# Kernel tuning notes

Measured on AMD Instinct MI355X. Metric: run time of the kernel, lower is better.

## Reference

```python
import jax, jax.numpy as jnp
import numpy as np

GB_TAU = 1.0
_NOISE_KEY = jax.random.key(42)


def setup_inputs() -> dict:
    key = jax.random.key(0)
    kq, kk, kv = jax.random.split(key, 3)
    n_genes, n_latent, d_k, n_cells = 16384, 4096, 64, 1024
    query = jax.random.normal(kq, (n_genes, d_k), dtype=jnp.float32)
    key_t = jax.random.normal(kk, (n_latent, d_k), dtype=jnp.float32)
    value = jax.random.normal(kv, (n_latent, n_cells), dtype=jnp.float32)
    return {"query": query, "key": key_t, "value": value}


def _gumbel_noise(shape, dtype):
    # standard Gumbel(0,1): -log(-log(U)), U ~ Uniform(0,1)
    u = jax.random.uniform(_NOISE_KEY, shape, dtype=dtype,
                           minval=jnp.finfo(dtype).tiny, maxval=1.0)
    return -jnp.log(-jnp.log(u))


def reference(query, key, value):
    d_k = query.shape[-1]
    # [n_genes, n_latent] scaled dot-product scores
    scores = jnp.matmul(query, key.T) / jnp.sqrt(jnp.asarray(d_k, query.dtype))
    # gumbel_softmax(hard=False): softmax((logits + g) / tau, axis=-1)
    g = _gumbel_noise(scores.shape, scores.dtype)
    p_attn = jax.nn.softmax((scores + g) / GB_TAU, axis=-1)
    out = jnp.matmul(p_attn, value)  # [n_genes, n_cells]
    return out, p_attn
```

## Files before the change

kernel.cpp:

```cpp
#include <hip/hip_runtime.h>
#include <cstdint>
#include <cstddef>

#define N_GENES  16384
#define N_LATENT 4096
#define D_K      64
#define N_CELLS  1024

#define NOISE_PARTITIONABLE 1

typedef __attribute__((ext_vector_type(8))) short bf16x8;
typedef __attribute__((ext_vector_type(4))) float f32x4;

__device__ __forceinline__ uint32_t rotl32(uint32_t x, int r) {
  return __builtin_amdgcn_alignbit(x, x, 32 - r);
}

__device__ __forceinline__ void threefry2x32(uint32_t c0, uint32_t c1,
                                             uint32_t& o0, uint32_t& o1) {
  const uint32_t ks0 = 0u, ks1 = 42u, ks2 = 0u ^ 42u ^ 0x1BD11BDAu;
  uint32_t x0 = c0 + ks0;
  uint32_t x1 = c1 + ks1;
#define TFR(r) { x0 += x1; x1 = rotl32(x1, r); x1 ^= x0; }
  TFR(13) TFR(15) TFR(26) TFR(6)
  x0 += ks1; x1 += ks2 + 1u;
  TFR(17) TFR(29) TFR(16) TFR(24)
  x0 += ks2; x1 += ks0 + 2u;
  TFR(13) TFR(15) TFR(26) TFR(6)
  x0 += ks0; x1 += ks1 + 3u;
  TFR(17) TFR(29) TFR(16) TFR(24)
  x0 += ks1; x1 += ks2 + 4u;
  TFR(13) TFR(15) TFR(26) TFR(6)
  x0 += ks2; x1 += ks0 + 5u;
#undef TFR
  o0 = x0; o1 = x1;
}

__device__ __forceinline__ uint32_t rand_bits(uint32_t m) {
#if NOISE_PARTITIONABLE
  uint32_t b0, b1;
  threefry2x32(0u, m, b0, b1);
  return b0 ^ b1;
#else
  const uint32_t h = 1u << 25;
  uint32_t b0, b1;
  if (m < h) { threefry2x32(m, m + h, b0, b1); return b0; }
  else       { threefry2x32(m - h, m, b0, b1); return b1; }
#endif
}

__device__ __forceinline__ float fastlog(float x) {
  float r;
  asm("v_log_f32 %0, %1" : "=v"(r) : "v"(x));
  return r * 0.69314718055994531f;
}

__device__ __forceinline__ float gumbel_noise(uint32_t m) {
  uint32_t bits = rand_bits(m);
  float f = __uint_as_float((bits >> 9) | 0x3f800000u) - 1.0f;
  float u = f + 1.17549435e-38f;
  float t = -fastlog(u);
  return -fastlog(t);
}

__device__ __forceinline__ ushort f2bf(float x) {
  uint32_t u = __float_as_uint(x);
  uint32_t r = (u + 0x7FFFu + ((u >> 16) & 1u)) >> 16;
  return (ushort)r;
}

__device__ __forceinline__ float bf2f(uint32_t us) {
  return __uint_as_float(us << 16);
}

__device__ __forceinline__ uint32_t cvtpk_bf16(float lo, float hi) {
  uint32_t r;
  asm("v_cvt_pk_bf16_f32 %0, %1, %2" : "=v"(r) : "v"(lo), "v"(hi));
  return r;
}

__device__ __forceinline__ int swz(int row, int kcol) {
  return row * 64 + (((kcol >> 3) ^ (row & 7)) << 3) + (kcol & 7);
}

__global__ __launch_bounds__(256) void k_logexp(const float* __restrict__ Q,
                                                const float* __restrict__ Kk,
                                                ushort* __restrict__ Pe,
                                                float* __restrict__ Sp) {
  __shared__ ushort Qh[64 * 64], Ql[64 * 64], Kh[64 * 64], Kl[64 * 64];
  const int t = threadIdx.x;
  const int bm = blockIdx.x, bn = blockIdx.y;
  const float4* Q4 = (const float4*)(Q + ((size_t)bm << 12));
  const float4* K4 = (const float4*)(Kk + ((size_t)bn << 12));
#pragma unroll
  for (int i = 0; i < 4; ++i) {
    int idx = t + (i << 8);
    int r = idx >> 4;
    int k0 = (idx & 15) << 2;
    int sidx = swz(r, k0);
    float4 a = Q4[idx];
    a.x *= 0.125f; a.y *= 0.125f; a.z *= 0.125f; a.w *= 0.125f;
    {
      uint32_t h01 = cvtpk_bf16(a.x, a.y), h23 = cvtpk_bf16(a.z, a.w);
      float lx = a.x - __uint_as_float(h01 << 16);
      float ly = a.y - __uint_as_float(h01 & 0xffff0000u);
      float lz = a.z - __uint_as_float(h23 << 16);
      float lw = a.w - __uint_as_float(h23 & 0xffff0000u);
      uint32_t l01 = cvtpk_bf16(lx, ly), l23 = cvtpk_bf16(lz, lw);
      *(uint2*)&Qh[sidx] = make_uint2(h01, h23);
      *(uint2*)&Ql[sidx] = make_uint2(l01, l23);
    }
    float4 b = K4[idx];
    {
      uint32_t h01 = cvtpk_bf16(b.x, b.y), h23 = cvtpk_bf16(b.z, b.w);
      float lx = b.x - __uint_as_float(h01 << 16);
      float ly = b.y - __uint_as_float(h01 & 0xffff0000u);
      float lz = b.z - __uint_as_float(h23 << 16);
      float lw = b.w - __uint_as_float(h23 & 0xffff0000u);
      uint32_t l01 = cvtpk_bf16(lx, ly), l23 = cvtpk_bf16(lz, lw);
      *(uint2*)&Kh[sidx] = make_uint2(h01, h23);
      *(uint2*)&Kl[sidx] = make_uint2(l01, l23);
    }
  }
  __syncthreads();

  const int l = t & 63, w = t >> 6;
  const int wm = (w >> 1) << 5, wn = (w & 1) << 5;
  const int fr = l & 15;
  const int seg = l >> 4;
  const int koff = seg << 3;
  f32x4 acc[2][2] = {};
#pragma unroll
  for (int kseg = 0; kseg < 2; ++kseg) {
    bf16x8 ah[2], al[2], bh[2], bl[2];
    const int kc = kseg * 32 + koff;
#pragma unroll
    for (int m = 0; m < 2; ++m) {
      int row = wm + m * 16 + fr;
      int sidx = swz(row, kc);
      ah[m] = *(const bf16x8*)&Qh[sidx];
      al[m] = *(const bf16x8*)&Ql[sidx];
    }
#pragma unroll
    for (int n = 0; n < 2; ++n) {
      int row = wn + n * 16 + fr;
      int sidx = swz(row, kc);
      bh[n] = *(const bf16x8*)&Kh[sidx];
      bl[n] = *(const bf16x8*)&Kl[sidx];
    }
#pragma unroll
    for (int m = 0; m < 2; ++m)
#pragma unroll
      for (int n = 0; n < 2; ++n) {
        acc[m][n] = __builtin_amdgcn_mfma_f32_16x16x32_bf16(
            ah[m], bh[n], acc[m][n], 0, 0, 0);
        acc[m][n] = __builtin_amdgcn_mfma_f32_16x16x32_bf16(
            ah[m], bl[n], acc[m][n], 0, 0, 0);
        acc[m][n] = __builtin_amdgcn_mfma_f32_16x16x32_bf16(
            al[m], bh[n], acc[m][n], 0, 0, 0);
      }
  }

  const float LOG2E = 1.44269504088896340f;
  const float NLN2 = -0.69314718055994531f;
  const int gr0 = (bm << 6) + wm + (seg << 2);
  const int gc0 = (bn << 6) + wn + fr;
  float sloc[2][4] = {};
#pragma unroll
  for (int m = 0; m < 2; ++m)
#pragma unroll
    for (int n = 0; n < 2; ++n) {
      int col = gc0 + n * 16;
      uint32_t mbase = (uint32_t)(gr0 + m * 16) * 4096u + (uint32_t)col;
      float e[4];
#pragma unroll
      for (int j = 0; j < 4; ++j) {
        uint32_t bits = rand_bits(mbase + (uint32_t)j * 4096u);
        float f = __uint_as_float((bits >> 9) | 0x3f800000u) - 1.0f;
        float u = f + 1.17549435e-38f;
        float lgu;
        asm("v_log_f32 %0, %1" : "=v"(lgu) : "v"(u));
        float tq = lgu * NLN2;
        float lgt;
        asm("v_log_f32 %0, %1" : "=v"(lgt) : "v"(tq));
        float ee;
        asm("v_exp_f32 %0, %1" : "=v"(ee)
            : "v"(fmaf(acc[m][n][j], LOG2E, -lgt)));
        e[j] = ee;
        sloc[m][j] += ee;
      }
      uint32_t p01 = cvtpk_bf16(e[0], e[1]);
      uint32_t p23 = cvtpk_bf16(e[2], e[3]);
      size_t base = (size_t)(gr0 + m * 16) * 4096 + col;
      Pe[base] = (ushort)p01;
      Pe[base + 4096] = (ushort)(p01 >> 16);
      Pe[base + 2 * 4096] = (ushort)p23;
      Pe[base + 3 * 4096] = (ushort)(p23 >> 16);
    }
  __shared__ float part[64][2];
#pragma unroll
  for (int m = 0; m < 2; ++m)
#pragma unroll
    for (int j = 0; j < 4; ++j) {
      float s = sloc[m][j];
      s += __shfl_xor(s, 1, 64); s += __shfl_xor(s, 2, 64);
      s += __shfl_xor(s, 4, 64); s += __shfl_xor(s, 8, 64);
      if (fr == 0) part[wm + m * 16 + (seg << 2) + j][wn >> 5] = s;
    }
  __syncthreads();
  if (t < 64)
    Sp[((size_t)(bm << 6) + t) * 64 + bn] = part[t][0] + part[t][1];
}

__global__ __launch_bounds__(256) void k_rowinv(const float* __restrict__ Sp,
                                                float* __restrict__ inv) {
  int r = blockIdx.x * 256 + threadIdx.x;
  const float4* s4 = (const float4*)(Sp + (size_t)r * 64);
  float s = 0.f;
#pragma unroll
  for (int i = 0; i < 16; ++i) {
    float4 v = s4[i];
    s += (v.x + v.y) + (v.z + v.w);
  }
  inv[r] = 1.0f / s;
}

__global__ __launch_bounds__(256) void k_vt(const float* __restrict__ V,
                                            ushort* __restrict__ VT) {
  __shared__ ushort tile[64][68];
  const int t = threadIdx.x;
  const int k0 = blockIdx.x << 6, n0 = blockIdx.y << 6;
#pragma unroll
  for (int i = 0; i < 16; ++i) {
    int idx = t + (i << 8);
    int kr = idx >> 6;
    int c = idx & 63;
    tile[c][kr] = f2bf(V[(size_t)(k0 + kr) * 1024 + n0 + c]);
  }
  __syncthreads();
#pragma unroll
  for (int i = 0; i < 8; ++i) {
    int idx = t + (i << 8);
    int n = idx >> 5, kp = idx & 31;
    ushort2 o;
    o.x = tile[n][2 * kp];
    o.y = tile[n][2 * kp + 1];
    ((ushort2*)&VT[(size_t)(n0 + n) * 4096 + k0])[kp] = o;
  }
}

__device__ __forceinline__ void llds16(void* lds, const void* g) {
  __builtin_amdgcn_global_load_lds(
      (const __attribute__((address_space(1))) uint32_t*)g,
      (__attribute__((address_space(3))) uint32_t*)lds, 16, 0, 0);
}

__device__ __forceinline__ void stage_kt(ushort* ldsA, ushort* ldsB,
                                         const ushort* gA, const ushort* gB,
                                         int t) {
#pragma unroll
  for (int i = 0; i < 4; ++i) {
    int cid = (i << 9) + t;
    int row = cid >> 3, g = cid & 7;
    int gs = g ^ (row & 7);
    llds16(ldsA + (size_t)cid * 8, gA + (size_t)row * 4096 + gs * 8);
  }
#pragma unroll
  for (int i = 0; i < 4; ++i) {
    int cid = (i << 9) + t;
    int row = cid >> 3, g = cid & 7;
    int gs = g ^ (row & 7);
    llds16(ldsB + (size_t)cid * 8, gB + (size_t)row * 4096 + gs * 8);
  }
}

__global__ __launch_bounds__(512, 2) void k_pv4(const ushort* __restrict__ Pe,
                                                const ushort* __restrict__ VT,
                                                const float* __restrict__ inv,
                                                float* __restrict__ P,
                                                float* __restrict__ O) {
  __shared__ ushort lds[2][2][256 * 64];
  const int t = threadIdx.x;
  const int b = blockIdx.x;
  const int xcd = b & 7, idx = b >> 3;
  const int by = xcd * 8 + (idx >> 2);
  const int bx = idx & 3;
  const int base_m = by << 8, base_n = bx << 8;
  const int l = t & 63, w = t >> 6;
  const int wm = w >> 2, wn = w & 3;
  const int fr = l & 15, seg = l >> 4;

  const ushort* gA = Pe + (size_t)base_m * 4096;
  const ushort* gB = VT + (size_t)base_n * 4096;

  const int pr_loc = bx * 64 + (t >> 3);
  const int pw_g = t & 7;
  const int pw_off = pr_loc * 64 + ((pw_g ^ (pr_loc & 7)) << 3);
  const int pw_row = base_m + pr_loc;
  const float iv_pw = inv[pw_row];
  float* Pdst = P + (size_t)pw_row * 4096 + pw_g * 8;

  f32x4 acc[8][4] = {};

  stage_kt(lds[0][0], lds[0][1], gA, gB, t);

#define LDA_H(mh)                                                            \
  {                                                                          \
    _Pragma("unroll") for (int m = 0; m < 4; ++m)                            \
        _Pragma("unroll") for (int kk = 0; kk < 2; ++kk) {                   \
      int row = wm * 128 + (mh)*64 + m * 16 + fr;                            \
      a[m][kk] = *(const bf16x8*)&A[row * 64 +                               \
                                    ((((kk << 2) + seg) ^ (row & 7)) << 3)]; \
    }                                                                        \
  }
#define LDB_H(dst, nh)                                                       \
  {                                                                          \
    _Pragma("unroll") for (int n = 0; n < 2; ++n)                            \
        _Pragma("unroll") for (int kk = 0; kk < 2; ++kk) {                   \
      int row = wn * 64 + (nh)*32 + n * 16 + fr;                             \
      dst[n][kk] = *(const bf16x8*)&B[row * 64 +                             \
                                    ((((kk << 2) + seg) ^ (row & 7)) << 3)]; \
    }                                                                        \
  }
#define QUADM(mh, nh, bb)                                                    \
  {                                                                          \
    __builtin_amdgcn_s_setprio(1);                                           \
    _Pragma("unroll") for (int m = 0; m < 4; ++m)                            \
        _Pragma("unroll") for (int n = 0; n < 2; ++n)                        \
            _Pragma("unroll") for (int kk = 0; kk < 2; ++kk)                 \
        acc[(mh)*4 + m][(nh)*2 + n] = __builtin_amdgcn_mfma_f32_16x16x32_bf16( \
            a[m][kk], bb[n][kk], acc[(mh)*4 + m][(nh)*2 + n], 0, 0, 0);      \
    __builtin_amdgcn_s_setprio(0);                                           \
  }

  for (int it = 0; it < 64; ++it) {
    const int slot = it & 1;
    const int ktn = (it < 63) ? it + 1 : it;
    stage_kt(lds[slot ^ 1][0], lds[slot ^ 1][1],
             gA + ktn * 64, gB + ktn * 64, t);
    asm volatile("s_waitcnt vmcnt(8)" ::: "memory");
    __builtin_amdgcn_s_barrier();
    const ushort* A = lds[slot][0];
    const ushort* B = lds[slot][1];
    bf16x8 a[4][2], b0[2][2], b1[2][2];
    LDA_H(0) LDB_H(b0, 0)
    QUADM(0, 0, b0)
    __builtin_amdgcn_s_barrier();
    LDB_H(b1, 1)
    QUADM(0, 1, b1)
    __builtin_amdgcn_s_barrier();
    LDA_H(1)
    QUADM(1, 0, b0)
    __builtin_amdgcn_s_barrier();
    QUADM(1, 1, b1)
    {
      bf16x8 pv_ = *(const bf16x8*)&A[pw_off];
      const uint32_t* pu = (const uint32_t*)&pv_;
      float4 o0, o1;
      uint32_t w0 = pu[0], w1 = pu[1], w2 = pu[2], w3 = pu[3];
      o0.x = bf2f(w0) * iv_pw;        o0.y = bf2f(w0 >> 16) * iv_pw;
      o0.z = bf2f(w1) * iv_pw;        o0.w = bf2f(w1 >> 16) * iv_pw;
      o1.x = bf2f(w2) * iv_pw;        o1.y = bf2f(w2 >> 16) * iv_pw;
      o1.z = bf2f(w3) * iv_pw;        o1.w = bf2f(w3 >> 16) * iv_pw;
      *(float4*)(Pdst + (size_t)it * 64) = o0;
      *(float4*)(Pdst + (size_t)it * 64 + 4) = o1;
    }
    __builtin_amdgcn_s_barrier();
  }

#pragma unroll
  for (int mi = 0; mi < 8; ++mi) {
    int row_ = base_m + wm * 128 + mi * 16 + seg * 4;
#pragma unroll
    for (int j = 0; j < 4; ++j) {
      float iv = inv[row_ + j];
#pragma unroll
      for (int ni = 0; ni < 4; ++ni)
        O[(size_t)(row_ + j) * 1024 + base_n + wn * 64 + ni * 16 + fr] =
            acc[mi][ni][j] * iv;
    }
  }
#undef LDA_H
#undef LDB_H
#undef QUADM
}

__global__ __launch_bounds__(256) void k_logits_raw(const float* __restrict__ Q,
                                                    const float* __restrict__ Kk,
                                                    float* __restrict__ L) {
  __shared__ float Qt[64][68];
  __shared__ float Kt[64][68];
  const int t = threadIdx.x;
  const int bm = blockIdx.x, bn = blockIdx.y;
  const float4* Q4 = (const float4*)(Q + ((size_t)bm << 12));
  const float4* K4 = (const float4*)(Kk + ((size_t)bn << 12));
#pragma unroll
  for (int i = 0; i < 4; ++i) {
    int idx = t + (i << 8);
    int r = idx >> 4;
    int k0 = (idx & 15) << 2;
    float4 a = Q4[idx];
    Qt[k0 + 0][r] = a.x; Qt[k0 + 1][r] = a.y;
    Qt[k0 + 2][r] = a.z; Qt[k0 + 3][r] = a.w;
    float4 b = K4[idx];
    Kt[k0 + 0][r] = b.x; Kt[k0 + 1][r] = b.y;
    Kt[k0 + 2][r] = b.z; Kt[k0 + 3][r] = b.w;
  }
  __syncthreads();
  const int r0 = (t >> 4) << 2;
  const int c0 = (t & 15) << 2;
  float acc[4][4] = {};
#pragma unroll 8
  for (int k = 0; k < 64; ++k) {
    float a[4], b[4];
    *(float4*)a = *(const float4*)&Qt[k][r0];
    *(float4*)b = *(const float4*)&Kt[k][c0];
#pragma unroll
    for (int i = 0; i < 4; ++i)
#pragma unroll
      for (int j = 0; j < 4; ++j)
        acc[i][j] = fmaf(a[i], b[j], acc[i][j]);
  }
  const int gr = (bm << 6) + r0;
  const int gc = (bn << 6) + c0;
#pragma unroll
  for (int i = 0; i < 4; ++i) {
    uint32_t mb = (uint32_t)(gr + i) * 4096u + (uint32_t)gc;
    float4 o;
    o.x = acc[i][0] * 0.125f + gumbel_noise(mb + 0u);
    o.y = acc[i][1] * 0.125f + gumbel_noise(mb + 1u);
    o.z = acc[i][2] * 0.125f + gumbel_noise(mb + 2u);
    o.w = acc[i][3] * 0.125f + gumbel_noise(mb + 3u);
    *(float4*)&L[(size_t)(gr + i) * 4096 + gc] = o;
  }
}

__global__ __launch_bounds__(256) void k_softmax(float* __restrict__ P) {
  const int row = blockIdx.x;
  float* Lr = P + ((size_t)row << 12);
  const int t = threadIdx.x;
  float4 v[4];
#pragma unroll
  for (int i = 0; i < 4; ++i) v[i] = ((const float4*)Lr)[t + (i << 8)];
  float mx = -3.402823466e38f;
#pragma unroll
  for (int i = 0; i < 4; ++i)
    mx = fmaxf(mx, fmaxf(fmaxf(v[i].x, v[i].y), fmaxf(v[i].z, v[i].w)));
#pragma unroll
  for (int o = 1; o < 64; o <<= 1) mx = fmaxf(mx, __shfl_xor(mx, o, 64));
  __shared__ float redm[4];
  __shared__ float reds[4];
  const int lane = t & 63, w = t >> 6;
  if (lane == 0) redm[w] = mx;
  __syncthreads();
  mx = fmaxf(fmaxf(redm[0], redm[1]), fmaxf(redm[2], redm[3]));
  float s = 0.f;
#pragma unroll
  for (int i = 0; i < 4; ++i) {
    v[i].x = expf(v[i].x - mx); v[i].y = expf(v[i].y - mx);
    v[i].z = expf(v[i].z - mx); v[i].w = expf(v[i].w - mx);
    s += (v[i].x + v[i].y) + (v[i].z + v[i].w);
  }
#pragma unroll
  for (int o = 1; o < 64; o <<= 1) s += __shfl_xor(s, o, 64);
  if (lane == 0) reds[w] = s;
  __syncthreads();
  const float inv = 1.0f / (((reds[0] + reds[1]) + (reds[2] + reds[3])));
#pragma unroll
  for (int i = 0; i < 4; ++i) {
    v[i].x *= inv; v[i].y *= inv; v[i].z *= inv; v[i].w *= inv;
    ((float4*)Lr)[t + (i << 8)] = v[i];
  }
}

__global__ __launch_bounds__(256) void k_pv(const float* __restrict__ P,
                                            const float* __restrict__ V,
                                            float* __restrict__ O) {
  __shared__ float Pt[32][132];
  __shared__ float Vs[32][132];
  const int t = threadIdx.x;
  const int base_m = blockIdx.x << 7;
  const int base_n = blockIdx.y << 7;
  const int tr = (t >> 4) << 2;
  const int tc = (t & 15) << 2;
  float acc[2][2][4][4] = {};
  for (int k0 = 0; k0 < N_LATENT; k0 += 32) {
#pragma unroll
    for (int i = 0; i < 4; ++i) {
      int idx = t + (i << 8);
      int m = idx >> 3;
      int kk = (idx & 7) << 2;
      float4 a = *(const float4*)&P[(size_t)(base_m + m) * 4096 + (k0 + kk)];
      Pt[kk + 0][m] = a.x; Pt[kk + 1][m] = a.y;
      Pt[kk + 2][m] = a.z; Pt[kk + 3][m] = a.w;
      int kv = idx >> 5;
      int n4 = (idx & 31) << 2;
      *(float4*)&Vs[kv][n4] =
          *(const float4*)&V[(size_t)(k0 + kv) * 1024 + base_n + n4];
    }
    __syncthreads();
#pragma unroll 4
    for (int k = 0; k < 32; ++k) {
      float a[2][4], b[2][4];
      *(float4*)a[0] = *(const float4*)&Pt[k][tr];
      *(float4*)a[1] = *(const float4*)&Pt[k][tr + 64];
      *(float4*)b[0] = *(const float4*)&Vs[k][tc];
      *(float4*)b[1] = *(const float4*)&Vs[k][tc + 64];
#pragma unroll
      for (int ih = 0; ih < 2; ++ih)
#pragma unroll
        for (int jh = 0; jh < 2; ++jh)
#pragma unroll
          for (int i = 0; i < 4; ++i)
#pragma unroll
            for (int j = 0; j < 4; ++j)
              acc[ih][jh][i][j] =
                  fmaf(a[ih][i], b[jh][j], acc[ih][jh][i][j]);
    }
    __syncthreads();
  }
#pragma unroll
  for (int ih = 0; ih < 2; ++ih)
#pragma unroll
    for (int i = 0; i < 4; ++i) {
      int row = base_m + (ih << 6) + tr + i;
#pragma unroll
      for (int jh = 0; jh < 2; ++jh) {
        float4 o;
        o.x = acc[ih][jh][i][0]; o.y = acc[ih][jh][i][1];
        o.z = acc[ih][jh][i][2]; o.w = acc[ih][jh][i][3];
        *(float4*)&O[(size_t)row * 1024 + base_n + (jh << 6) + tc] = o;
      }
    }
}

extern "C" void kernel_launch(void* const* d_in, const int* in_sizes, int n_in,
                              void* d_out, int out_size, void* d_ws, size_t ws_size,
                              hipStream_t stream) {
  const float* Q = (const float*)d_in[0];
  const float* K = (const float*)d_in[1];
  const float* V = (const float*)d_in[2];
  float* O = (float*)d_out;
  float* P = O + (size_t)N_GENES * N_CELLS;

  const size_t pe_bytes = (size_t)N_GENES * N_LATENT * 2;
  const size_t vt_bytes = (size_t)N_CELLS * N_LATENT * 2;
  const size_t inv_bytes = (size_t)N_GENES * 4;
  const bool fast = ws_size >= pe_bytes + vt_bytes + inv_bytes;

  if (fast) {
    ushort* Pe = (ushort*)d_ws;
    ushort* VT = (ushort*)((char*)d_ws + pe_bytes);
    float* inv = (float*)((char*)d_ws + pe_bytes + vt_bytes);
    float* Sp = P;

    k_logexp<<<dim3(N_GENES / 64, N_LATENT / 64), 256, 0, stream>>>(Q, K, Pe, Sp);
    k_rowinv<<<N_GENES / 256, 256, 0, stream>>>(Sp, inv);
    k_vt<<<dim3(N_LATENT / 64, N_CELLS / 64), 256, 0, stream>>>(V, VT);
    k_pv4<<<256, 512, 0, stream>>>(Pe, VT, inv, P, O);
  } else {
    k_logits_raw<<<dim3(N_GENES / 64, N_LATENT / 64), 256, 0, stream>>>(Q, K, P);
    k_softmax<<<N_GENES, 256, 0, stream>>>(P);
    k_pv<<<dim3(N_GENES / 128, N_CELLS / 128), 256, 0, stream>>>(P, V, O);
  }
}
```

Baseline: 357.7 us.

## Interleave next-tile global-to-LDS loads across MFMA quadrants in PV kernel

The next K-tile's A and B global-to-LDS loads in the PV GEMM are now split into four half-tile issues, one placed between each MFMA quadrant, instead of all being issued at the top of the iteration. The aim is to spread memory traffic through the compute phase and replace the vmcnt(8) wait with a tighter wait at the start of the next iteration. This adds more barriers per iteration and a full drain before the loop begins, and it depends on the fp32 P stores not disturbing the vmcnt accounting.

```diff
diff --git a/kernel.cpp b/kernel.cpp
--- a/kernel.cpp
+++ b/kernel.cpp
@@ -255,26 +255,31 @@
       (__attribute__((address_space(3))) uint32_t*)lds, 16, 0, 0);
 }
 
-__device__ __forceinline__ void stage_kt(ushort* ldsA, ushort* ldsB,
-                                         const ushort* gA, const ushort* gB,
-                                         int t) {
+__device__ __forceinline__ void stage_full(ushort* ldsS, const ushort* gS,
+                                           int t) {
 #pragma unroll
   for (int i = 0; i < 4; ++i) {
     int cid = (i << 9) + t;
     int row = cid >> 3, g = cid & 7;
     int gs = g ^ (row & 7);
-    llds16(ldsA + (size_t)cid * 8, gA + (size_t)row * 4096 + gs * 8);
-  }
-#pragma unroll
-  for (int i = 0; i < 4; ++i) {
+    llds16(ldsS + (size_t)cid * 8, gS + (size_t)row * 4096 + gs * 8);
+  }
+}
+
+__device__ __forceinline__ void stage_half(ushort* ldsS, const ushort* gS,
+                                           int rowoff, int t) {
+#pragma unroll
+  for (int i = 0; i < 2; ++i) {
     int cid = (i << 9) + t;
-    int row = cid >> 3, g = cid & 7;
+    int row = rowoff + (cid >> 3);
+    int g = cid & 7;
     int gs = g ^ (row & 7);
-    llds16(ldsB + (size_t)cid * 8, gB + (size_t)row * 4096 + gs * 8);
-  }
-}
-
-__global__ __launch_bounds__(512, 2) void k_pv4(const ushort* __restrict__ Pe,
+    llds16(ldsS + ((size_t)row * 8 + g) * 8,
+           gS + (size_t)row * 4096 + gs * 8);
+  }
+}
+
+__global__ __launch_bounds__(512, 2) void k_pv5(const ushort* __restrict__ Pe,
                                                 const ushort* __restrict__ VT,
                                                 const float* __restrict__ inv,
                                                 float* __restrict__ P,
@@ -302,7 +307,10 @@
 
   f32x4 acc[8][4] = {};
 
-  stage_kt(lds[0][0], lds[0][1], gA, gB, t);
+  stage_full(lds[0][0], gA, t);
+  stage_full(lds[0][1], gB, t);
+  asm volatile("s_waitcnt vmcnt(0)" ::: "memory");
+  __builtin_amdgcn_s_barrier();
 
 #define LDA_H(mh)                                                            \
   {                                                                          \
@@ -335,22 +343,33 @@
 
   for (int it = 0; it < 64; ++it) {
     const int slot = it & 1;
-    const int ktn = (it < 63) ? it + 1 : it;
-    stage_kt(lds[slot ^ 1][0], lds[slot ^ 1][1],
-             gA + ktn * 64, gB + ktn * 64, t);
-    asm volatile("s_waitcnt vmcnt(8)" ::: "memory");
-    __builtin_amdgcn_s_barrier();
     const ushort* A = lds[slot][0];
     const ushort* B = lds[slot][1];
+    ushort* An = lds[slot ^ 1][0];
+    ushort* Bn = lds[slot ^ 1][1];
+    const ushort* gAn = gA + (it + 1) * 64;
+    const ushort* gBn = gB + (it + 1) * 64;
+    if (it > 0) {
+      asm volatile("s_waitcnt vmcnt(2)" ::: "memory");
+      __builtin_amdgcn_s_barrier();
+    }
     bf16x8 a[4][2], b0[2][2], b1[2][2];
     LDA_H(0) LDB_H(b0, 0)
+    if (it < 63) stage_half(An, gAn, 0, t);
+    __builtin_amdgcn_s_barrier();
     QUADM(0, 0, b0)
     __builtin_amdgcn_s_barrier();
     LDB_H(b1, 1)
+    if (it < 63) stage_half(An, gAn, 128, t);
+    __builtin_amdgcn_s_barrier();
     QUADM(0, 1, b1)
     __builtin_amdgcn_s_barrier();
     LDA_H(1)
+    if (it < 63) stage_half(Bn, gBn, 0, t);
+    __builtin_amdgcn_s_barrier();
     QUADM(1, 0, b0)
+    __builtin_amdgcn_s_barrier();
+    if (it < 63) stage_half(Bn, gBn, 128, t);
     __builtin_amdgcn_s_barrier();
     QUADM(1, 1, b1)
     {
@@ -557,7 +576,7 @@
     k_logexp<<<dim3(N_GENES / 64, N_LATENT / 64), 256, 0, stream>>>(Q, K, Pe, Sp);
     k_rowinv<<<N_GENES / 256, 256, 0, stream>>>(Sp, inv);
     k_vt<<<dim3(N_LATENT / 64, N_CELLS / 64), 256, 0, stream>>>(V, VT);
-    k_pv4<<<256, 512, 0, stream>>>(Pe, VT, inv, P, O);
+    k_pv5<<<256, 512, 0, stream>>>(Pe, VT, inv, P, O);
   } else {
     k_logits_raw<<<dim3(N_GENES / 64, N_LATENT / 64), 256, 0, stream>>>(Q, K, P);
     k_softmax<<<N_GENES, 256, 0, stream>>>(P);
```

Result: faster. 337.6 us (-5.6%).

## Retile PV GEMM to 128x128 blocks with 256 threads and restructured pipeline

Applied to the files above, without the earlier changes.

Replaces the 256x256-tile, 512-thread PV kernel with a 128x128-tile, 256-thread kernel launched over 1024 blocks. Each wave now computes a 64x64 sub-tile, and the block-to-XCD mapping is remapped. The double-buffer pipeline is also changed: it waits for the current tile, then issues the next tile's loads after the barrier. In k_logexp, the row-sum scratch buffer now reuses the Ql LDS buffer, which needs an extra barrier. The aim is better occupancy and load balance across CUs, at the cost of more global reloads of Pe and VT, since smaller tiles give less operand reuse.

```diff
diff --git a/kernel.cpp b/kernel.cpp
--- a/kernel.cpp
+++ b/kernel.cpp
@@ -88,6 +88,7 @@
                                                 ushort* __restrict__ Pe,
                                                 float* __restrict__ Sp) {
   __shared__ ushort Qh[64 * 64], Ql[64 * 64], Kh[64 * 64], Kl[64 * 64];
+  float (*part)[2] = (float(*)[2])Ql;
   const int t = threadIdx.x;
   const int bm = blockIdx.x, bn = blockIdx.y;
   const float4* Q4 = (const float4*)(Q + ((size_t)bm << 12));
@@ -160,6 +161,7 @@
             al[m], bh[n], acc[m][n], 0, 0, 0);
       }
   }
+  __syncthreads();
 
   const float LOG2E = 1.44269504088896340f;
   const float NLN2 = -0.69314718055994531f;
@@ -197,7 +199,6 @@
       Pe[base + 2 * 4096] = (ushort)p23;
       Pe[base + 3 * 4096] = (ushort)(p23 >> 16);
     }
-  __shared__ float part[64][2];
 #pragma unroll
   for (int m = 0; m < 2; ++m)
 #pragma unroll
@@ -255,134 +256,115 @@
       (__attribute__((address_space(3))) uint32_t*)lds, 16, 0, 0);
 }
 
-__device__ __forceinline__ void stage_kt(ushort* ldsA, ushort* ldsB,
-                                         const ushort* gA, const ushort* gB,
+__device__ __forceinline__ void stage128(ushort* ldsS, const ushort* gS,
                                          int t) {
 #pragma unroll
   for (int i = 0; i < 4; ++i) {
-    int cid = (i << 9) + t;
+    int cid = (i << 8) + t;
     int row = cid >> 3, g = cid & 7;
     int gs = g ^ (row & 7);
-    llds16(ldsA + (size_t)cid * 8, gA + (size_t)row * 4096 + gs * 8);
-  }
-#pragma unroll
-  for (int i = 0; i < 4; ++i) {
-    int cid = (i << 9) + t;
-    int row = cid >> 3, g = cid & 7;
-    int gs = g ^ (row & 7);
-    llds16(ldsB + (size_t)cid * 8, gB + (size_t)row * 4096 + gs * 8);
-  }
-}
-
-__global__ __launch_bounds__(512, 2) void k_pv4(const ushort* __restrict__ Pe,
+    llds16(ldsS + (size_t)cid * 8, gS + (size_t)row * 4096 + gs * 8);
+  }
+}
+
+__global__ __launch_bounds__(256, 2) void k_pv6(const ushort* __restrict__ Pe,
                                                 const ushort* __restrict__ VT,
                                                 const float* __restrict__ inv,
                                                 float* __restrict__ P,
                                                 float* __restrict__ O) {
-  __shared__ ushort lds[2][2][256 * 64];
+  __shared__ ushort lds[2][2][128 * 64];
   const int t = threadIdx.x;
   const int b = blockIdx.x;
-  const int xcd = b & 7, idx = b >> 3;
-  const int by = xcd * 8 + (idx >> 2);
-  const int bx = idx & 3;
-  const int base_m = by << 8, base_n = bx << 8;
+  const int Lb = (b & 7) * 128 + (b >> 3);
+  const int by = Lb >> 3, bx = Lb & 7;
+  const int base_m = by << 7, base_n = bx << 7;
   const int l = t & 63, w = t >> 6;
-  const int wm = w >> 2, wn = w & 3;
+  const int wm = (w >> 1) << 6, wn = (w & 1) << 6;
   const int fr = l & 15, seg = l >> 4;
 
   const ushort* gA = Pe + (size_t)base_m * 4096;
   const ushort* gB = VT + (size_t)base_n * 4096;
 
-  const int pr_loc = bx * 64 + (t >> 3);
-  const int pw_g = t & 7;
-  const int pw_off = pr_loc * 64 + ((pw_g ^ (pr_loc & 7)) << 3);
+  const int pr_loc = (bx << 4) + (t >> 4);
+  const int pcg = t & 15;
+  const int pw_ldsoff = pr_loc * 64 + (((pcg >> 1) ^ (pr_loc & 7)) << 3) +
+                        (pcg & 1) * 4;
   const int pw_row = base_m + pr_loc;
   const float iv_pw = inv[pw_row];
-  float* Pdst = P + (size_t)pw_row * 4096 + pw_g * 8;
-
-  f32x4 acc[8][4] = {};
-
-  stage_kt(lds[0][0], lds[0][1], gA, gB, t);
-
-#define LDA_H(mh)                                                            \
-  {                                                                          \
-    _Pragma("unroll") for (int m = 0; m < 4; ++m)                            \
-        _Pragma("unroll") for (int kk = 0; kk < 2; ++kk) {                   \
-      int row = wm * 128 + (mh)*64 + m * 16 + fr;                            \
-      a[m][kk] = *(const bf16x8*)&A[row * 64 +                               \
-                                    ((((kk << 2) + seg) ^ (row & 7)) << 3)]; \
-    }                                                                        \
-  }
-#define LDB_H(dst, nh)                                                       \
-  {                                                                          \
-    _Pragma("unroll") for (int n = 0; n < 2; ++n)                            \
-        _Pragma("unroll") for (int kk = 0; kk < 2; ++kk) {                   \
-      int row = wn * 64 + (nh)*32 + n * 16 + fr;                             \
-      dst[n][kk] = *(const bf16x8*)&B[row * 64 +                             \
-                                    ((((kk << 2) + seg) ^ (row & 7)) << 3)]; \
-    }                                                                        \
-  }
-#define QUADM(mh, nh, bb)                                                    \
-  {                                                                          \
-    __builtin_amdgcn_s_setprio(1);                                           \
-    _Pragma("unroll") for (int m = 0; m < 4; ++m)                            \
-        _Pragma("unroll") for (int n = 0; n < 2; ++n)                        \
-            _Pragma("unroll") for (int kk = 0; kk < 2; ++kk)                 \
-        acc[(mh)*4 + m][(nh)*2 + n] = __builtin_amdgcn_mfma_f32_16x16x32_bf16( \
-            a[m][kk], bb[n][kk], acc[(mh)*4 + m][(nh)*2 + n], 0, 0, 0);      \
-    __builtin_amdgcn_s_setprio(0);                                           \
-  }
+  float* Pdst = P + (size_t)pw_row * 4096 + pcg * 4;
+
+  f32x4 acc[4][4] = {};
+
+  stage128(lds[0][0], gA, t);
+  stage128(lds[0][1], gB, t);
+  asm volatile("s_waitcnt vmcnt(0)" ::: "memory");
+  __builtin_amdgcn_s_barrier();
 
   for (int it = 0; it < 64; ++it) {
     const int slot = it & 1;
-    const int ktn = (it < 63) ? it + 1 : it;
-    stage_kt(lds[slot ^ 1][0], lds[slot ^ 1][1],
-             gA + ktn * 64, gB + ktn * 64, t);
-    asm volatile("s_waitcnt vmcnt(8)" ::: "memory");
-    __builtin_amdgcn_s_barrier();
+    if (it > 0) {
+      asm volatile("s_waitcnt vmcnt(1)" ::: "memory");
+      __builtin_amdgcn_s_barrier();
+    }
     const ushort* A = lds[slot][0];
     const ushort* B = lds[slot][1];
-    bf16x8 a[4][2], b0[2][2], b1[2][2];
-    LDA_H(0) LDB_H(b0, 0)
-    QUADM(0, 0, b0)
+    if (it < 63) {
+      stage128(lds[slot ^ 1][0], gA + (it + 1) * 64, t);
+      stage128(lds[slot ^ 1][1], gB + (it + 1) * 64, t);
+    }
+    bf16x8 a[4][2], bb[4][2];
+#pragma unroll
+    for (int mi = 0; mi < 4; ++mi)
+#pragma unroll
+      for (int kk = 0; kk < 2; ++kk) {
+        int row = wm + mi * 16 + fr;
+        a[mi][kk] = *(const bf16x8*)
+            &A[row * 64 + ((((kk << 2) + seg) ^ (row & 7)) << 3)];
+      }
+#pragma unroll
+    for (int ni = 0; ni < 4; ++ni)
+#pragma unroll
+      for (int kk = 0; kk < 2; ++kk) {
+        int row = wn + ni * 16 + fr;
+        bb[ni][kk] = *(const bf16x8*)
+            &B[row * 64 + ((((kk << 2) + seg) ^ (row & 7)) << 3)];
+      }
+    __builtin_amdgcn_s_setprio(1);
+#pragma unroll
+    for (int kk = 0; kk < 2; ++kk)
+#pragma unroll
+      for (int mi = 0; mi < 4; ++mi)
+#pragma unroll
+        for (int ni = 0; ni < 4; ++ni)
+          acc[mi][ni] = __builtin_amdgcn_mfma_f32_16x16x32_bf16(
+              a[mi][kk], bb[ni][kk], acc[mi][ni], 0, 0, 0);
+    __builtin_amdgcn_s_setprio(0);
+    {
+      uint2 pw = *(const uint2*)&A[pw_ldsoff];
+      float4 o;
+      o.x = bf2f(pw.x & 0xFFFFu) * iv_pw;
+      o.y = bf2f(pw.x >> 16) * iv_pw;
+      o.z = bf2f(pw.y & 0xFFFFu) * iv_pw;
+      o.w = bf2f(pw.y >> 16) * iv_pw;
+      *(float4*)(Pdst + (size_t)it * 64) = o;
+    }
     __builtin_amdgcn_s_barrier();
-    LDB_H(b1, 1)
-    QUADM(0, 1, b1)
-    __builtin_amdgcn_s_barrier();
-    LDA_H(1)
-    QUADM(1, 0, b0)
-    __builtin_amdgcn_s_barrier();
-    QUADM(1, 1, b1)
-    {
-      bf16x8 pv_ = *(const bf16x8*)&A[pw_off];
-      const uint32_t* pu = (const uint32_t*)&pv_;
-      float4 o0, o1;
-      uint32_t w0 = pu[0], w1 = pu[1], w2 = pu[2], w3 = pu[3];
-      o0.x = bf2f(w0) * iv_pw;        o0.y = bf2f(w0 >> 16) * iv_pw;
-      o0.z = bf2f(w1) * iv_pw;        o0.w = bf2f(w1 >> 16) * iv_pw;
-      o1.x = bf2f(w2) * iv_pw;        o1.y = bf2f(w2 >> 16) * iv_pw;
-      o1.z = bf2f(w3) * iv_pw;        o1.w = bf2f(w3 >> 16) * iv_pw;
-      *(float4*)(Pdst + (size_t)it * 64) = o0;
-      *(float4*)(Pdst + (size_t)it * 64 + 4) = o1;
-    }
-    __builtin_amdgcn_s_barrier();
-  }
-
-#pragma unroll
-  for (int mi = 0; mi < 8; ++mi) {
-    int row_ = base_m + wm * 128 + mi * 16 + seg * 4;
+  }
+
+  const int orow0 = base_m + wm + seg * 4;
+  const int ocol0 = base_n + wn + fr;
+#pragma unroll
+  for (int mi = 0; mi < 4; ++mi) {
+    int row_ = orow0 + mi * 16;
 #pragma unroll
     for (int j = 0; j < 4; ++j) {
       float iv = inv[row_ + j];
 #pragma unroll
       for (int ni = 0; ni < 4; ++ni)
-        O[(size_t)(row_ + j) * 1024 + base_n + wn * 64 + ni * 16 + fr] =
+        O[(size_t)(row_ + j) * 1024 + ocol0 + ni * 16] =
             acc[mi][ni][j] * iv;
     }
   }
-#undef LDA_H
-#undef LDB_H
-#undef QUADM
 }
 
 __global__ __launch_bounds__(256) void k_logits_raw(const float* __restrict__ Q,
@@ -557,7 +539,7 @@
     k_logexp<<<dim3(N_GENES / 64, N_LATENT / 64), 256, 0, stream>>>(Q, K, Pe, Sp);
     k_rowinv<<<N_GENES / 256, 256, 0, stream>>>(Sp, inv);
     k_vt<<<dim3(N_LATENT / 64, N_CELLS / 64), 256, 0, stream>>>(V, VT);
-    k_pv4<<<256, 512, 0, stream>>>(Pe, VT, inv, P, O);
+    k_pv6<<<(N_GENES / 128) * (N_CELLS / 128), 256, 0, stream>>>(Pe, VT, inv, P, O);
   } else {
     k_logits_raw<<<dim3(N_GENES / 64, N_LATENT / 64), 256, 0, stream>>>(Q, K, P);
     k_softmax<<<N_GENES, 256, 0, stream>>>(P);
```

Measured after the change: 387.4 us. 1.08x slower.
